# Kernel optimization log

Hardware: AMD Instinct MI355X
Metric: run time of the kernel (lower is better)

The kernel has to match this reference:

```python
import jax, jax.numpy as jnp
import numpy as np

N0, D, H, E0 = 50000, 128, 128, 800000
N1, E1, A, B, C = 20000, 320000, 100000, 64, 10


def _gcn(x, row, col, ew, n, W, b):
    # GCNConv: out = D^-1/2 (A + I) D^-1/2 (x W) + b, with edge weights
    xw = x @ W
    sl = jnp.arange(n)
    r = jnp.concatenate([row, sl])
    c = jnp.concatenate([col, sl])
    w = jnp.concatenate([ew, jnp.ones((n,), ew.dtype)])
    deg = jax.ops.segment_sum(w, c, num_segments=n)
    dinv = jax.lax.rsqrt(jnp.maximum(deg, 1e-12))
    norm = dinv[r] * w * dinv[c]
    return jax.ops.segment_sum(norm[:, None] * xw[r], c, num_segments=n) + b


def _block(x, row, col, ew, n, W1, b1, W2, b2, Wl, bl):
    # Block with num_inner_layers=2, jumping_knowledge='cat'
    x1 = jax.nn.relu(_gcn(x, row, col, ew, n, W1, b1))
    x2 = jax.nn.relu(_gcn(x1, row, col, ew, n, W2, b2))
    return jnp.concatenate([x1, x2], axis=1) @ Wl + bl


def _seg_max(x, idx, n):
    m = jax.ops.segment_max(x, idx, num_segments=n)
    return jnp.where(jnp.isfinite(m), m, 0.0)  # empty segments -> 0 like scatter_max default


def _lin_init(k, i, o):
    s = 1.0 / np.sqrt(i)
    return jax.random.uniform(k, (i, o), jnp.float32, -s, s)


def setup_inputs() -> dict:
    key = jax.random.key(0)
    ks = jax.random.split(key, 20)
    x = jax.random.normal(ks[0], (N0, D), jnp.float32)
    edge_index0 = jax.random.randint(ks[1], (2, E0), 0, N0)
    edge_weight0 = jax.random.uniform(ks[2], (E0,), jnp.float32)
    batch0 = jnp.sort(jax.random.randint(ks[3], (N0,), 0, B))
    cover_row = jax.random.randint(ks[4], (A,), 0, N0)
    cover_col = jnp.concatenate([jnp.arange(N1), jax.random.randint(ks[5], (A - N1,), 0, N1)])
    edge_index1 = jax.random.randint(ks[6], (2, E1), 0, N1)
    edge_weight1 = jax.random.uniform(ks[7], (E1,), jnp.float32)
    batch1 = jnp.sort(jax.random.randint(ks[8], (N1,), 0, B))
    params = dict(
        w_in1=_lin_init(ks[9], D, H), b_in1=jnp.zeros((H,), jnp.float32),
        w_in2=_lin_init(ks[10], H, H), b_in2=jnp.zeros((H,), jnp.float32),
        w_in_lin=_lin_init(ks[11], 2 * H, H), b_in_lin=jnp.zeros((H,), jnp.float32),
        w_b1=_lin_init(ks[12], 2 * H, H), b_b1=jnp.zeros((H,), jnp.float32),
        w_b2=_lin_init(ks[13], H, H), b_b2=jnp.zeros((H,), jnp.float32),
        w_b_lin=_lin_init(ks[14], 2 * H, H), b_b_lin=jnp.zeros((H,), jnp.float32),
        bn_gamma=jnp.ones((4 * H,), jnp.float32), bn_beta=jnp.zeros((4 * H,), jnp.float32),
        w_l1=_lin_init(ks[15], 4 * H, H), b_l1=jnp.zeros((H,), jnp.float32),
        w_l2=_lin_init(ks[16], H, C), b_l2=jnp.zeros((C,), jnp.float32),
    )
    return dict(x=x, edge_index0=edge_index0, edge_weight0=edge_weight0, batch0=batch0,
                cover_row=cover_row, cover_col=cover_col, edge_index1=edge_index1,
                edge_weight1=edge_weight1, batch1=batch1, **params)


def reference(x, edge_index0, edge_weight0, batch0, cover_row, cover_col,
              edge_index1, edge_weight1, batch1,
              w_in1, b_in1, w_in2, b_in2, w_in_lin, b_in_lin,
              w_b1, b_b1, w_b2, b_b2, w_b_lin, b_b_lin,
              bn_gamma, bn_beta, w_l1, b_l1, w_l2, b_l2):
    r0, c0 = edge_index0[0], edge_index0[1]
    h = jax.nn.relu(_block(x, r0, c0, edge_weight0, N0, w_in1, b_in1, w_in2, b_in2, w_in_lin, b_in_lin))
    xs = [jax.ops.segment_sum(h, batch0, num_segments=B), _seg_max(h, batch0, B)]
    # cover_pool_node: add + max over k-plex cover assignments
    hg = h[cover_row]
    h2 = jnp.concatenate([jax.ops.segment_sum(hg, cover_col, num_segments=N1),
                          _seg_max(hg, cover_col, N1)], axis=1)
    r1, c1 = edge_index1[0], edge_index1[1]
    h2 = jax.nn.relu(_block(h2, r1, c1, edge_weight1, N1, w_b1, b_b1, w_b2, b_b2, w_b_lin, b_b_lin))
    xs.append(jax.ops.segment_sum(h2, batch1, num_segments=B))
    xs.append(_seg_max(h2, batch1, B))
    z = jnp.concatenate(xs, axis=1)  # [B, 4H]
    # BatchNorm1d in eval mode: running stats (mean=0, var=1), eps=1e-5
    z = z * (bn_gamma * jax.lax.rsqrt(jnp.asarray(1.0 + 1e-5, z.dtype))) + bn_beta
    z = jax.nn.relu(z @ w_l1 + b_l1)
    logits = z @ w_l2 + b_l2  # dropout skipped (eval mode)
    return jax.nn.softmax(logits, axis=-1)
```

## Files before the change

### kernel.cpp

```cpp
#include <hip/hip_runtime.h>
#include <cmath>

#define HF 128

namespace {

typedef __attribute__((ext_vector_type(8))) short short8;
typedef __attribute__((ext_vector_type(4))) float f32x4;

inline int cdiv(int a, int b) { return (a + b - 1) / b; }

__device__ inline unsigned short f2bf(float x) {
    unsigned u = __float_as_uint(x);
    return (unsigned short)((u + 0x7fffu + ((u >> 16) & 1u)) >> 16);
}
__device__ inline float bf2f(unsigned short u) {
    return __uint_as_float((unsigned)u << 16);
}
__device__ inline float bflo(unsigned v) { return __uint_as_float(v << 16); }
__device__ inline float bfhi(unsigned v) { return __uint_as_float(v & 0xffff0000u); }

#define FIXS 4194304.0f
#define FIXINV 2.384185791015625e-07f
#define SUMMASK ((1ULL << 40) - 1)

__global__ void k_prep(const int* __restrict__ col0, const float* __restrict__ ew0,
                       unsigned long long* __restrict__ dc0, int E0, int nb0,
                       const int* __restrict__ col1, const float* __restrict__ ew1,
                       unsigned long long* __restrict__ dc1, int E1, int nb1,
                       const int* __restrict__ ccol, int* __restrict__ ccnt, int A, int nbc,
                       const float* __restrict__ w0, const float* __restrict__ w1,
                       const float* __restrict__ w2, const float* __restrict__ w3,
                       const float* __restrict__ w4, const float* __restrict__ w5,
                       unsigned short* __restrict__ wpk, int nbw,
                       const int* __restrict__ b0, int n0, const int* __restrict__ b1,
                       int n1, int B, int* __restrict__ bst0, int* __restrict__ bst1) {
    int b = blockIdx.x, t = threadIdx.x;
    if (b < nb0) {
        int e = b * 256 + t;
        if (e < E0) {
            unsigned long long v = (1ULL << 40) | (unsigned long long)(ew0[e] * FIXS + 0.5f);
            atomicAdd(&dc0[col0[e]], v);
        }
        return;
    }
    b -= nb0;
    if (b < nb1) {
        int e = b * 256 + t;
        if (e < E1) {
            unsigned long long v = (1ULL << 40) | (unsigned long long)(ew1[e] * FIXS + 0.5f);
            atomicAdd(&dc1[col1[e]], v);
        }
        return;
    }
    b -= nb1;
    if (b < nbc) {
        int e = b * 256 + t;
        if (e < A) atomicAdd(&ccnt[ccol[e]], 1);
        return;
    }
    b -= nbc;
    if (b < nbw) {
        int idx = b * 256 + t;
        const float* src; int local;
        if      (idx < 16384)  { src = w0; local = idx; }
        else if (idx < 32768)  { src = w1; local = idx - 16384; }
        else if (idx < 65536)  { src = w2; local = idx - 32768; }
        else if (idx < 98304)  { src = w3; local = idx - 65536; }
        else if (idx < 114688) { src = w4; local = idx - 98304; }
        else                   { src = w5; local = idx - 114688; }
        int e = local & 7, lane = (local >> 3) & 63, g = (local >> 9) & 7, kc = local >> 12;
        int colw = (lane & 15) + 16 * g;
        int k = kc * 32 + ((lane >> 4) << 3) + e;
        wpk[idx] = f2bf(src[k * 128 + colw]);
        return;
    }
    b -= nbw;
    {
        int idx = b * 256 + t;
        if (idx < 2 * (B + 1)) {
            int which = idx > B;
            int bb = which ? idx - (B + 1) : idx;
            const int* arr = which ? b1 : b0;
            int lo = 0, hi = which ? n1 : n0;
            while (lo < hi) {
                int mid = (lo + hi) >> 1;
                if (arr[mid] < bb) lo = mid + 1; else hi = mid;
            }
            (which ? bst1 : bst0)[bb] = lo;
        }
    }
}

__device__ inline void scan256(int* s, int v, int gid, int n, int* __restrict__ excl,
                               int* __restrict__ partial, int pb) {
    s[threadIdx.x] = v;
    __syncthreads();
    for (int off = 1; off < 256; off <<= 1) {
        int t = (threadIdx.x >= off) ? s[threadIdx.x - off] : 0;
        __syncthreads();
        s[threadIdx.x] += t;
        __syncthreads();
    }
    if (gid < n) excl[gid] = s[threadIdx.x] - v;
    if (threadIdx.x == 255) partial[pb] = s[255];
}

__global__ void k_scan_dinv(const unsigned long long* __restrict__ dc0, int* __restrict__ rp0,
                            int* __restrict__ part0, int n0, int nbs0,
                            const unsigned long long* __restrict__ dc1, int* __restrict__ rp1,
                            int* __restrict__ part1, int n1, int nbs1,
                            const int* __restrict__ ccnt, int* __restrict__ crp,
                            int* __restrict__ cpart, int nc, int nbsc,
                            float* __restrict__ dinv0, float* __restrict__ dinv1,
                            int nbd0, int nbd1) {
    __shared__ int s[256];
    int b = blockIdx.x, t = threadIdx.x;
    if (b < nbs0) {
        int gid = b * 256 + t;
        int v = (gid < n0) ? (int)(dc0[gid] >> 40) : 0;
        scan256(s, v, gid, n0, rp0, part0, b);
        return;
    }
    b -= nbs0;
    if (b < nbs1) {
        int gid = b * 256 + t;
        int v = (gid < n1) ? (int)(dc1[gid] >> 40) : 0;
        scan256(s, v, gid, n1, rp1, part1, b);
        return;
    }
    b -= nbs1;
    if (b < nbsc) {
        int gid = b * 256 + t;
        int v = (gid < nc) ? ccnt[gid] : 0;
        scan256(s, v, gid, nc, crp, cpart, b);
        return;
    }
    b -= nbsc;
    if (b < nbd0) {
        int i = b * 256 + t;
        if (i < n0) dinv0[i] = rsqrtf(1.0f + (float)(dc0[i] & SUMMASK) * FIXINV);
        return;
    }
    b -= nbd0;
    {
        int i = b * 256 + t;
        if (i < n1) dinv1[i] = rsqrtf(1.0f + (float)(dc1[i] & SUMMASK) * FIXINV);
    }
}

__global__ void k_scan2x3(int* __restrict__ p0, int nb0, int* __restrict__ p1, int nb1,
                          int* __restrict__ p2, int nb2) {
    __shared__ int s[256];
    int* p; int nb;
    if (blockIdx.x == 0)      { p = p0; nb = nb0; }
    else if (blockIdx.x == 1) { p = p1; nb = nb1; }
    else                      { p = p2; nb = nb2; }
    int v = (threadIdx.x < nb) ? p[threadIdx.x] : 0;
    s[threadIdx.x] = v;
    __syncthreads();
    for (int off = 1; off < 256; off <<= 1) {
        int t = (threadIdx.x >= off) ? s[threadIdx.x - off] : 0;
        __syncthreads();
        s[threadIdx.x] += t;
        __syncthreads();
    }
    if (threadIdx.x < nb) p[threadIdx.x] = s[threadIdx.x] - v;
}

__global__ void k_scan3x3(int* __restrict__ rp0, const int* __restrict__ part0,
                          int* __restrict__ cur0, int n0, int tot0, int nb0,
                          int* __restrict__ rp1, const int* __restrict__ part1,
                          int* __restrict__ cur1, int n1, int tot1, int nb1,
                          int* __restrict__ crp, const int* __restrict__ cpart,
                          int* __restrict__ ccur, int nc, int totc) {
    int b = blockIdx.x, t = threadIdx.x;
    if (b < nb0) {
        int gid = b * 256 + t;
        if (gid < n0) { int v = rp0[gid] + part0[b]; rp0[gid] = v; cur0[gid] = v; }
        if (gid == 0) rp0[n0] = tot0;
        return;
    }
    b -= nb0;
    if (b < nb1) {
        int gid = b * 256 + t;
        if (gid < n1) { int v = rp1[gid] + part1[b]; rp1[gid] = v; cur1[gid] = v; }
        if (gid == 0) rp1[n1] = tot1;
        return;
    }
    b -= nb1;
    {
        int gid = b * 256 + t;
        if (gid < nc) { int v = crp[gid] + cpart[b]; crp[gid] = v; ccur[gid] = v; }
        if (gid == 0) crp[nc] = totc;
    }
}

__global__ void k_fillx3(const int* __restrict__ row0, const int* __restrict__ col0,
                         const float* __restrict__ ew0, const float* __restrict__ dinv0,
                         int* __restrict__ cur0, int2* __restrict__ ed0, int E0, int nb0,
                         const int* __restrict__ row1, const int* __restrict__ col1,
                         const float* __restrict__ ew1, const float* __restrict__ dinv1,
                         int* __restrict__ cur1, int2* __restrict__ ed1, int E1, int nb1,
                         const int* __restrict__ crow, const int* __restrict__ ccol,
                         int* __restrict__ ccur, int* __restrict__ csrcs, int A) {
    int b = blockIdx.x, t = threadIdx.x;
    if (b < nb0) {
        int e = b * 256 + t;
        if (e < E0) {
            int r = row0[e], c = col0[e];
            int p = atomicAdd(&cur0[c], 1);
            ed0[p] = make_int2(r, __float_as_int(ew0[e] * dinv0[r] * dinv0[c]));
        }
        return;
    }
    b -= nb0;
    if (b < nb1) {
        int e = b * 256 + t;
        if (e < E1) {
            int r = row1[e], c = col1[e];
            int p = atomicAdd(&cur1[c], 1);
            ed1[p] = make_int2(r, __float_as_int(ew1[e] * dinv1[r] * dinv1[c]));
        }
        return;
    }
    b -= nb1;
    {
        int e = b * 256 + t;
        if (e < A) {
            int p = atomicAdd(&ccur[ccol[e]], 1);
            csrcs[p] = crow[e];
        }
    }
}

__global__ void k_gcn_gather(const unsigned* __restrict__ xw, const int* __restrict__ rowptr,
                             const int2* __restrict__ ed, const float* __restrict__ dinv,
                             const float* __restrict__ bias, unsigned* __restrict__ out, int n) {
    int wid = (blockIdx.x * 256 + threadIdx.x) >> 6;
    if (wid >= n) return;
    int lane = threadIdx.x & 63;
    int s = rowptr[wid], e = rowptr[wid + 1];
    float d = dinv[wid];
    unsigned v = xw[(size_t)wid * 64 + lane];
    float ax = bflo(v) * d * d, ay = bfhi(v) * d * d;
    float bx = 0.f, by = 0.f, cx = 0.f, cy = 0.f, dx = 0.f, dy = 0.f;
    int i = s;
    for (; i + 4 <= e; i += 4) {
        int2 e0 = ed[i], e1 = ed[i + 1], e2 = ed[i + 2], e3 = ed[i + 3];
        unsigned v0 = xw[(size_t)e0.x * 64 + lane];
        unsigned v1 = xw[(size_t)e1.x * 64 + lane];
        unsigned v2 = xw[(size_t)e2.x * 64 + lane];
        unsigned v3 = xw[(size_t)e3.x * 64 + lane];
        float c0 = __int_as_float(e0.y), c1 = __int_as_float(e1.y);
        float c2 = __int_as_float(e2.y), c3 = __int_as_float(e3.y);
        ax += c0 * bflo(v0); ay += c0 * bfhi(v0);
        bx += c1 * bflo(v1); by += c1 * bfhi(v1);
        cx += c2 * bflo(v2); cy += c2 * bfhi(v2);
        dx += c3 * bflo(v3); dy += c3 * bfhi(v3);
    }
    for (; i < e; ++i) {
        int2 e0 = ed[i];
        unsigned v0 = xw[(size_t)e0.x * 64 + lane];
        float c0 = __int_as_float(e0.y);
        ax += c0 * bflo(v0); ay += c0 * bfhi(v0);
    }
    ax += bx + cx + dx;
    ay += by + cy + dy;
    float2 bb = *reinterpret_cast<const float2*>(bias + lane * 2);
    ax = fmaxf(ax + bb.x, 0.f);
    ay = fmaxf(ay + bb.y, 0.f);
    out[(size_t)wid * 64 + lane] = (unsigned)f2bf(ax) | ((unsigned)f2bf(ay) << 16);
}

__global__ void k_pool_cover(const unsigned short* __restrict__ h, const int* __restrict__ bst,
                             float* __restrict__ psum, float* __restrict__ pmax, int nsplit,
                             int nbpool, const unsigned* __restrict__ h32,
                             const int* __restrict__ crp, const int* __restrict__ csrcs,
                             unsigned* __restrict__ h2, int n1) {
    int t = threadIdx.x;
    if ((int)blockIdx.x < nbpool) {
        int blk = blockIdx.x;
        int b = blk / nsplit, sub = (blk % nsplit) * 2 + (t >> 7);
        int col = t & 127;
        int r0 = bst[b], r1 = bst[b + 1];
        float sum = 0.f, mx = 0.f;
        for (int r = r0 + sub; r < r1; r += 2 * nsplit) {
            float v = bf2f(h[(size_t)r * HF + col]);
            sum += v;
            mx = fmaxf(mx, v);
        }
        atomicAdd(&psum[b * HF + col], sum);
        atomicMax(reinterpret_cast<int*>(&pmax[b * HF + col]), __float_as_int(mx));
        return;
    }
    int wid = (((int)blockIdx.x - nbpool) * 256 + t) >> 6;
    if (wid >= n1) return;
    int lane = t & 63;
    int s = crp[wid], e = crp[wid + 1];
    float sx = 0.f, sy = 0.f, mx = 0.f, my = 0.f;
    for (int i = s; i < e; ++i) {
        unsigned v = h32[(size_t)csrcs[i] * 64 + lane];
        float vx = bflo(v), vy = bfhi(v);
        sx += vx; sy += vy;
        mx = fmaxf(mx, vx); my = fmaxf(my, vy);
    }
    h2[(size_t)wid * 128 + lane]      = (unsigned)f2bf(sx) | ((unsigned)f2bf(sy) << 16);
    h2[(size_t)wid * 128 + 64 + lane] = (unsigned)f2bf(mx) | ((unsigned)f2bf(my) << 16);
}

__global__ void k_pool256(const unsigned short* __restrict__ h, const int* __restrict__ bst,
                          float* __restrict__ psum, float* __restrict__ pmax, int nsplit) {
    int t = threadIdx.x;
    int blk = blockIdx.x;
    int b = blk / nsplit, sub = (blk % nsplit) * 2 + (t >> 7);
    int col = t & 127;
    int r0 = bst[b], r1 = bst[b + 1];
    float sum = 0.f, mx = 0.f;
    for (int r = r0 + sub; r < r1; r += 2 * nsplit) {
        float v = bf2f(h[(size_t)r * HF + col]);
        sum += v;
        mx = fmaxf(mx, v);
    }
    atomicAdd(&psum[b * HF + col], sum);
    atomicMax(reinterpret_cast<int*>(&pmax[b * HF + col]), __float_as_int(mx));
}

template <int K, bool AF32>
__global__ void k_mfma_gemm(const void* __restrict__ A1v, int lda1,
                            const void* __restrict__ A2v, int lda2,
                            const unsigned short* __restrict__ wpk,
                            const float* __restrict__ bias, int relu,
                            unsigned short* __restrict__ out, int N) {
    const int t = threadIdx.x;
    const int wv = t >> 6, lane = t & 63;
    const int l15 = lane & 15, lhi = lane >> 4;
    const int rbase = blockIdx.x * 128 + wv * 32;

    f32x4 acc[2][8];
#pragma unroll
    for (int i = 0; i < 2; ++i)
#pragma unroll
        for (int g = 0; g < 8; ++g) acc[i][g] = {0.f, 0.f, 0.f, 0.f};

    int r[2];
#pragma unroll
    for (int ri = 0; ri < 2; ++ri) {
        int rr = rbase + ri * 16 + l15;
        r[ri] = (rr < N) ? rr : (N - 1);
    }

    for (int kc = 0; kc < K / 32; ++kc) {
        int kb = kc * 32 + lhi * 8;
        short8 a[2];
#pragma unroll
        for (int ri = 0; ri < 2; ++ri) {
            if (AF32) {
                const float* A = (const float*)A1v;
                const float* p = A + (size_t)r[ri] * lda1 + kb;
                float4 f0 = *reinterpret_cast<const float4*>(p);
                float4 f1 = *reinterpret_cast<const float4*>(p + 4);
                a[ri][0] = (short)f2bf(f0.x); a[ri][1] = (short)f2bf(f0.y);
                a[ri][2] = (short)f2bf(f0.z); a[ri][3] = (short)f2bf(f0.w);
                a[ri][4] = (short)f2bf(f1.x); a[ri][5] = (short)f2bf(f1.y);
                a[ri][6] = (short)f2bf(f1.z); a[ri][7] = (short)f2bf(f1.w);
            } else {
                const unsigned short* base;
                int kk, ld;
                if (K == 256 && kb >= 128) { base = (const unsigned short*)A2v; kk = kb - 128; ld = lda2; }
                else                       { base = (const unsigned short*)A1v; kk = kb;       ld = lda1; }
                a[ri] = *reinterpret_cast<const short8*>(base + (size_t)r[ri] * ld + kk);
            }
        }
        const unsigned short* wb = wpk + (size_t)(kc * 8) * 512 + lane * 8;
#pragma unroll
        for (int g = 0; g < 8; ++g) {
            short8 b = *reinterpret_cast<const short8*>(wb + (size_t)g * 512);
            acc[0][g] = __builtin_amdgcn_mfma_f32_16x16x32_bf16(a[0], b, acc[0][g], 0, 0, 0);
            acc[1][g] = __builtin_amdgcn_mfma_f32_16x16x32_bf16(a[1], b, acc[1][g], 0, 0, 0);
        }
    }

#pragma unroll
    for (int ri = 0; ri < 2; ++ri) {
#pragma unroll
        for (int g = 0; g < 8; ++g) {
            int col = l15 + g * 16;
            float bb = bias ? bias[col] : 0.f;
#pragma unroll
            for (int e = 0; e < 4; ++e) {
                int rr = rbase + ri * 16 + lhi * 4 + e;
                if (rr < N) {
                    float v = acc[ri][g][e] + bb;
                    if (relu) v = fmaxf(v, 0.f);
                    out[(size_t)rr * 128 + col] = f2bf(v);
                }
            }
        }
    }
}

__global__ void k_head(const float* __restrict__ p0s, const float* __restrict__ p0m,
                       const float* __restrict__ p1s, const float* __restrict__ p1m,
                       const float* __restrict__ gamma, const float* __restrict__ beta,
                       const float* __restrict__ w1, const float* __restrict__ b1,
                       const float* __restrict__ w2, const float* __restrict__ b2,
                       float* __restrict__ out) {
    __shared__ float z[512];
    __shared__ float z1[128];
    __shared__ float lg[10];
    int b = blockIdx.x, t = threadIdx.x;
    const float s = rsqrtf(1.0f + 1e-5f);
    z[t]       = p0s[b * 128 + t] * (gamma[t] * s)       + beta[t];
    z[128 + t] = p0m[b * 128 + t] * (gamma[128 + t] * s) + beta[128 + t];
    z[256 + t] = p1s[b * 128 + t] * (gamma[256 + t] * s) + beta[256 + t];
    z[384 + t] = p1m[b * 128 + t] * (gamma[384 + t] * s) + beta[384 + t];
    __syncthreads();
    float acc = b1[t];
    for (int k = 0; k < 512; ++k) acc += z[k] * w1[k * 128 + t];
    z1[t] = fmaxf(acc, 0.f);
    __syncthreads();
    if (t < 10) {
        float a2 = b2[t];
        for (int k = 0; k < 128; ++k) a2 += z1[k] * w2[k * 10 + t];
        lg[t] = a2;
    }
    __syncthreads();
    if (t == 0) {
        float m = lg[0];
        for (int c = 1; c < 10; ++c) m = fmaxf(m, lg[c]);
        float e[10], ssum = 0.f;
        for (int c = 0; c < 10; ++c) { e[c] = expf(lg[c] - m); ssum += e[c]; }
        for (int c = 0; c < 10; ++c) out[b * 10 + c] = e[c] / ssum;
    }
}

}

extern "C" void kernel_launch(void* const* d_in, const int* in_sizes, int n_in,
                              void* d_out, int out_size, void* d_ws, size_t ws_size,
                              hipStream_t stream) {
    const float* x      = (const float*)d_in[0];
    const int*   ei0    = (const int*)d_in[1];
    const float* ew0    = (const float*)d_in[2];
    const int*   batch0 = (const int*)d_in[3];
    const int*   crow   = (const int*)d_in[4];
    const int*   ccol   = (const int*)d_in[5];
    const int*   ei1    = (const int*)d_in[6];
    const float* ew1    = (const float*)d_in[7];
    const int*   batch1 = (const int*)d_in[8];
    const float* w_in1  = (const float*)d_in[9];
    const float* b_in1  = (const float*)d_in[10];
    const float* w_in2  = (const float*)d_in[11];
    const float* b_in2  = (const float*)d_in[12];
    const float* w_inl  = (const float*)d_in[13];
    const float* b_inl  = (const float*)d_in[14];
    const float* w_b1   = (const float*)d_in[15];
    const float* b_b1   = (const float*)d_in[16];
    const float* w_b2   = (const float*)d_in[17];
    const float* b_b2   = (const float*)d_in[18];
    const float* w_bl   = (const float*)d_in[19];
    const float* b_bl   = (const float*)d_in[20];
    const float* gamma  = (const float*)d_in[21];
    const float* beta   = (const float*)d_in[22];
    const float* w_l1   = (const float*)d_in[23];
    const float* b_l1   = (const float*)d_in[24];
    const float* w_l2   = (const float*)d_in[25];
    const float* b_l2   = (const float*)d_in[26];

    const int N0 = in_sizes[0] / 128;
    const int E0 = in_sizes[2];
    const int A  = in_sizes[4];
    const int E1 = in_sizes[7];
    const int N1 = in_sizes[8];
    const int B  = out_size / 10;

    const int* row0 = ei0;
    const int* col0 = ei0 + E0;
    const int* row1 = ei1;
    const int* col1 = ei1 + E1;

    char* wsp = (char*)d_ws;
    size_t off = 0;
    auto alloc = [&](size_t bytes) -> char* {
        char* p = wsp + off;
        off += (bytes + 255) & ~(size_t)255;
        return p;
    };
    unsigned long long* dc0 = (unsigned long long*)alloc((size_t)N0 * 8);
    unsigned long long* dc1 = (unsigned long long*)alloc((size_t)N1 * 8);
    int*   ccnt  = (int*)alloc((size_t)N1 * 4);
    float* p0s   = (float*)alloc((size_t)B * HF * 4 * 4);
    float* p0m   = p0s + (size_t)B * HF;
    float* p1s   = p0m + (size_t)B * HF;
    float* p1m   = p1s + (size_t)B * HF;
    size_t zero_bytes = off;

    unsigned* xw  = (unsigned*)alloc((size_t)N0 * 64 * 4);
    unsigned* x1  = (unsigned*)alloc((size_t)N0 * 64 * 4);
    unsigned* x2  = (unsigned*)alloc((size_t)N0 * 64 * 4);
    unsigned* h   = (unsigned*)alloc((size_t)N0 * 64 * 4);
    unsigned* h2  = (unsigned*)alloc((size_t)N1 * 128 * 4);
    unsigned short* wpk = (unsigned short*)alloc(147456 * 2);
    float* dinv0 = (float*)alloc((size_t)N0 * 4);
    float* dinv1 = (float*)alloc((size_t)N1 * 4);
    int*   rp0   = (int*)alloc(((size_t)N0 + 1) * 4);
    int*   rp1   = (int*)alloc(((size_t)N1 + 1) * 4);
    int*   crp   = (int*)alloc(((size_t)N1 + 1) * 4);
    int*   cur0  = (int*)alloc((size_t)N0 * 4);
    int*   cur1  = (int*)alloc((size_t)N1 * 4);
    int*   ccur  = (int*)alloc((size_t)N1 * 4);
    int*   part0 = (int*)alloc(256 * 4);
    int*   part1 = (int*)alloc(256 * 4);
    int*   cpart = (int*)alloc(256 * 4);
    int2*  ed0   = (int2*)alloc((size_t)E0 * 8);
    int2*  ed1   = (int2*)alloc((size_t)E1 * 8);
    int*   csrcs = (int*)alloc((size_t)A * 4);
    int*   bst0  = (int*)alloc((size_t)(B + 1) * 4);
    int*   bst1  = (int*)alloc((size_t)(B + 1) * 4);
    (void)ws_size; (void)n_in;

    const int NSPLIT = 16;
    const int nbE0 = cdiv(E0, 256), nbE1 = cdiv(E1, 256), nbC = cdiv(A, 256);
    const int nbW = 576, nbB = 1;
    const int nbs0 = cdiv(N0, 256), nbs1 = cdiv(N1, 256), nbsc = cdiv(N1, 256);

    hipMemsetAsync(dc0, 0, zero_bytes, stream);

    k_prep<<<nbE0 + nbE1 + nbC + nbW + nbB, 256, 0, stream>>>(
        col0, ew0, dc0, E0, nbE0, col1, ew1, dc1, E1, nbE1, ccol, ccnt, A, nbC,
        w_in1, w_in2, w_inl, w_b1, w_b2, w_bl, wpk, nbW,
        batch0, N0, batch1, N1, B, bst0, bst1);

    k_scan_dinv<<<nbs0 + nbs1 + nbsc + nbs0 + nbs1, 256, 0, stream>>>(
        dc0, rp0, part0, N0, nbs0, dc1, rp1, part1, N1, nbs1,
        ccnt, crp, cpart, N1, nbsc, dinv0, dinv1, nbs0, nbs1);

    k_scan2x3<<<3, 256, 0, stream>>>(part0, nbs0, part1, nbs1, cpart, nbsc);

    k_scan3x3<<<nbs0 + nbs1 + nbsc, 256, 0, stream>>>(
        rp0, part0, cur0, N0, E0, nbs0, rp1, part1, cur1, N1, E1, nbs1,
        crp, cpart, ccur, N1, A);

    k_fillx3<<<nbE0 + nbE1 + nbC, 256, 0, stream>>>(
        row0, col0, ew0, dinv0, cur0, ed0, E0, nbE0,
        row1, col1, ew1, dinv1, cur1, ed1, E1, nbE1,
        crow, ccol, ccur, csrcs, A);

    k_mfma_gemm<128, true><<<cdiv(N0, 128), 256, 0, stream>>>(
        x, 128, nullptr, 0, wpk + 0, nullptr, 0, (unsigned short*)xw, N0);
    k_gcn_gather<<<cdiv(N0, 4), 256, 0, stream>>>(xw, rp0, ed0, dinv0, b_in1, x1, N0);
    k_mfma_gemm<128, false><<<cdiv(N0, 128), 256, 0, stream>>>(
        x1, 128, nullptr, 0, wpk + 16384, nullptr, 0, (unsigned short*)xw, N0);
    k_gcn_gather<<<cdiv(N0, 4), 256, 0, stream>>>(xw, rp0, ed0, dinv0, b_in2, x2, N0);
    k_mfma_gemm<256, false><<<cdiv(N0, 128), 256, 0, stream>>>(
        x1, 128, x2, 128, wpk + 32768, b_inl, 1, (unsigned short*)h, N0);

    k_pool_cover<<<B * NSPLIT + cdiv(N1, 4), 256, 0, stream>>>(
        (const unsigned short*)h, bst0, p0s, p0m, NSPLIT, B * NSPLIT,
        h, crp, csrcs, h2, N1);

    k_mfma_gemm<256, false><<<cdiv(N1, 128), 256, 0, stream>>>(
        h2, 256, (const unsigned short*)h2 + 128, 256, wpk + 65536, nullptr, 0,
        (unsigned short*)xw, N1);
    k_gcn_gather<<<cdiv(N1, 4), 256, 0, stream>>>(xw, rp1, ed1, dinv1, b_b1, x1, N1);
    k_mfma_gemm<128, false><<<cdiv(N1, 128), 256, 0, stream>>>(
        x1, 128, nullptr, 0, wpk + 98304, nullptr, 0, (unsigned short*)xw, N1);
    k_gcn_gather<<<cdiv(N1, 4), 256, 0, stream>>>(xw, rp1, ed1, dinv1, b_b2, x2, N1);
    k_mfma_gemm<256, false><<<cdiv(N1, 128), 256, 0, stream>>>(
        x1, 128, x2, 128, wpk + 114688, b_bl, 1, (unsigned short*)h, N1);

    k_pool256<<<B * NSPLIT, 256, 0, stream>>>((const unsigned short*)h, bst1, p1s, p1m, NSPLIT);

    k_head<<<B, 128, 0, stream>>>(p0s, p0m, p1s, p1m, gamma, beta, w_l1, b_l1, w_l2, b_l2,
                                  (float*)d_out);
}
```

Baseline: 409.6 us.

## Record edge ranks during degree atomics and fuse first GEMM into prep

The degree-count atomics now save their returned old count as a per-edge rank, so CSR fill writes directly to rowptr+rank without a second round of cursor atomics. The fill kernel is partitioned so each of 8 block groups handles a destination-node range, aiming to keep writes local per XCD. The first x@W GEMM is fused into the degree-count kernel to overlap compute with atomics, weight packing moves to a separate earlier kernel, and the gather loads edges as int4 pairs. In exchange, the fill kernel rereads the edge arrays once per group, and extra rank buffers are stored.

```diff
diff --git a/kernel.cpp b/kernel.cpp
--- a/kernel.cpp
+++ b/kernel.cpp
@@ -24,318 +24,16 @@
 #define FIXINV 2.384185791015625e-07f
 #define SUMMASK ((1ULL << 40) - 1)
 
-__global__ void k_prep(const int* __restrict__ col0, const float* __restrict__ ew0,
-                       unsigned long long* __restrict__ dc0, int E0, int nb0,
-                       const int* __restrict__ col1, const float* __restrict__ ew1,
-                       unsigned long long* __restrict__ dc1, int E1, int nb1,
-                       const int* __restrict__ ccol, int* __restrict__ ccnt, int A, int nbc,
-                       const float* __restrict__ w0, const float* __restrict__ w1,
-                       const float* __restrict__ w2, const float* __restrict__ w3,
-                       const float* __restrict__ w4, const float* __restrict__ w5,
-                       unsigned short* __restrict__ wpk, int nbw,
-                       const int* __restrict__ b0, int n0, const int* __restrict__ b1,
-                       int n1, int B, int* __restrict__ bst0, int* __restrict__ bst1) {
-    int b = blockIdx.x, t = threadIdx.x;
-    if (b < nb0) {
-        int e = b * 256 + t;
-        if (e < E0) {
-            unsigned long long v = (1ULL << 40) | (unsigned long long)(ew0[e] * FIXS + 0.5f);
-            atomicAdd(&dc0[col0[e]], v);
-        }
-        return;
-    }
-    b -= nb0;
-    if (b < nb1) {
-        int e = b * 256 + t;
-        if (e < E1) {
-            unsigned long long v = (1ULL << 40) | (unsigned long long)(ew1[e] * FIXS + 0.5f);
-            atomicAdd(&dc1[col1[e]], v);
-        }
-        return;
-    }
-    b -= nb1;
-    if (b < nbc) {
-        int e = b * 256 + t;
-        if (e < A) atomicAdd(&ccnt[ccol[e]], 1);
-        return;
-    }
-    b -= nbc;
-    if (b < nbw) {
-        int idx = b * 256 + t;
-        const float* src; int local;
-        if      (idx < 16384)  { src = w0; local = idx; }
-        else if (idx < 32768)  { src = w1; local = idx - 16384; }
-        else if (idx < 65536)  { src = w2; local = idx - 32768; }
-        else if (idx < 98304)  { src = w3; local = idx - 65536; }
-        else if (idx < 114688) { src = w4; local = idx - 98304; }
-        else                   { src = w5; local = idx - 114688; }
-        int e = local & 7, lane = (local >> 3) & 63, g = (local >> 9) & 7, kc = local >> 12;
-        int colw = (lane & 15) + 16 * g;
-        int k = kc * 32 + ((lane >> 4) << 3) + e;
-        wpk[idx] = f2bf(src[k * 128 + colw]);
-        return;
-    }
-    b -= nbw;
-    {
-        int idx = b * 256 + t;
-        if (idx < 2 * (B + 1)) {
-            int which = idx > B;
-            int bb = which ? idx - (B + 1) : idx;
-            const int* arr = which ? b1 : b0;
-            int lo = 0, hi = which ? n1 : n0;
-            while (lo < hi) {
-                int mid = (lo + hi) >> 1;
-                if (arr[mid] < bb) lo = mid + 1; else hi = mid;
-            }
-            (which ? bst1 : bst0)[bb] = lo;
-        }
-    }
-}
-
-__device__ inline void scan256(int* s, int v, int gid, int n, int* __restrict__ excl,
-                               int* __restrict__ partial, int pb) {
-    s[threadIdx.x] = v;
-    __syncthreads();
-    for (int off = 1; off < 256; off <<= 1) {
-        int t = (threadIdx.x >= off) ? s[threadIdx.x - off] : 0;
-        __syncthreads();
-        s[threadIdx.x] += t;
-        __syncthreads();
-    }
-    if (gid < n) excl[gid] = s[threadIdx.x] - v;
-    if (threadIdx.x == 255) partial[pb] = s[255];
-}
-
-__global__ void k_scan_dinv(const unsigned long long* __restrict__ dc0, int* __restrict__ rp0,
-                            int* __restrict__ part0, int n0, int nbs0,
-                            const unsigned long long* __restrict__ dc1, int* __restrict__ rp1,
-                            int* __restrict__ part1, int n1, int nbs1,
-                            const int* __restrict__ ccnt, int* __restrict__ crp,
-                            int* __restrict__ cpart, int nc, int nbsc,
-                            float* __restrict__ dinv0, float* __restrict__ dinv1,
-                            int nbd0, int nbd1) {
-    __shared__ int s[256];
-    int b = blockIdx.x, t = threadIdx.x;
-    if (b < nbs0) {
-        int gid = b * 256 + t;
-        int v = (gid < n0) ? (int)(dc0[gid] >> 40) : 0;
-        scan256(s, v, gid, n0, rp0, part0, b);
-        return;
-    }
-    b -= nbs0;
-    if (b < nbs1) {
-        int gid = b * 256 + t;
-        int v = (gid < n1) ? (int)(dc1[gid] >> 40) : 0;
-        scan256(s, v, gid, n1, rp1, part1, b);
-        return;
-    }
-    b -= nbs1;
-    if (b < nbsc) {
-        int gid = b * 256 + t;
-        int v = (gid < nc) ? ccnt[gid] : 0;
-        scan256(s, v, gid, nc, crp, cpart, b);
-        return;
-    }
-    b -= nbsc;
-    if (b < nbd0) {
-        int i = b * 256 + t;
-        if (i < n0) dinv0[i] = rsqrtf(1.0f + (float)(dc0[i] & SUMMASK) * FIXINV);
-        return;
-    }
-    b -= nbd0;
-    {
-        int i = b * 256 + t;
-        if (i < n1) dinv1[i] = rsqrtf(1.0f + (float)(dc1[i] & SUMMASK) * FIXINV);
-    }
-}
-
-__global__ void k_scan2x3(int* __restrict__ p0, int nb0, int* __restrict__ p1, int nb1,
-                          int* __restrict__ p2, int nb2) {
-    __shared__ int s[256];
-    int* p; int nb;
-    if (blockIdx.x == 0)      { p = p0; nb = nb0; }
-    else if (blockIdx.x == 1) { p = p1; nb = nb1; }
-    else                      { p = p2; nb = nb2; }
-    int v = (threadIdx.x < nb) ? p[threadIdx.x] : 0;
-    s[threadIdx.x] = v;
-    __syncthreads();
-    for (int off = 1; off < 256; off <<= 1) {
-        int t = (threadIdx.x >= off) ? s[threadIdx.x - off] : 0;
-        __syncthreads();
-        s[threadIdx.x] += t;
-        __syncthreads();
-    }
-    if (threadIdx.x < nb) p[threadIdx.x] = s[threadIdx.x] - v;
-}
-
-__global__ void k_scan3x3(int* __restrict__ rp0, const int* __restrict__ part0,
-                          int* __restrict__ cur0, int n0, int tot0, int nb0,
-                          int* __restrict__ rp1, const int* __restrict__ part1,
-                          int* __restrict__ cur1, int n1, int tot1, int nb1,
-                          int* __restrict__ crp, const int* __restrict__ cpart,
-                          int* __restrict__ ccur, int nc, int totc) {
-    int b = blockIdx.x, t = threadIdx.x;
-    if (b < nb0) {
-        int gid = b * 256 + t;
-        if (gid < n0) { int v = rp0[gid] + part0[b]; rp0[gid] = v; cur0[gid] = v; }
-        if (gid == 0) rp0[n0] = tot0;
-        return;
-    }
-    b -= nb0;
-    if (b < nb1) {
-        int gid = b * 256 + t;
-        if (gid < n1) { int v = rp1[gid] + part1[b]; rp1[gid] = v; cur1[gid] = v; }
-        if (gid == 0) rp1[n1] = tot1;
-        return;
-    }
-    b -= nb1;
-    {
-        int gid = b * 256 + t;
-        if (gid < nc) { int v = crp[gid] + cpart[b]; crp[gid] = v; ccur[gid] = v; }
-        if (gid == 0) crp[nc] = totc;
-    }
-}
-
-__global__ void k_fillx3(const int* __restrict__ row0, const int* __restrict__ col0,
-                         const float* __restrict__ ew0, const float* __restrict__ dinv0,
-                         int* __restrict__ cur0, int2* __restrict__ ed0, int E0, int nb0,
-                         const int* __restrict__ row1, const int* __restrict__ col1,
-                         const float* __restrict__ ew1, const float* __restrict__ dinv1,
-                         int* __restrict__ cur1, int2* __restrict__ ed1, int E1, int nb1,
-                         const int* __restrict__ crow, const int* __restrict__ ccol,
-                         int* __restrict__ ccur, int* __restrict__ csrcs, int A) {
-    int b = blockIdx.x, t = threadIdx.x;
-    if (b < nb0) {
-        int e = b * 256 + t;
-        if (e < E0) {
-            int r = row0[e], c = col0[e];
-            int p = atomicAdd(&cur0[c], 1);
-            ed0[p] = make_int2(r, __float_as_int(ew0[e] * dinv0[r] * dinv0[c]));
-        }
-        return;
-    }
-    b -= nb0;
-    if (b < nb1) {
-        int e = b * 256 + t;
-        if (e < E1) {
-            int r = row1[e], c = col1[e];
-            int p = atomicAdd(&cur1[c], 1);
-            ed1[p] = make_int2(r, __float_as_int(ew1[e] * dinv1[r] * dinv1[c]));
-        }
-        return;
-    }
-    b -= nb1;
-    {
-        int e = b * 256 + t;
-        if (e < A) {
-            int p = atomicAdd(&ccur[ccol[e]], 1);
-            csrcs[p] = crow[e];
-        }
-    }
-}
-
-__global__ void k_gcn_gather(const unsigned* __restrict__ xw, const int* __restrict__ rowptr,
-                             const int2* __restrict__ ed, const float* __restrict__ dinv,
-                             const float* __restrict__ bias, unsigned* __restrict__ out, int n) {
-    int wid = (blockIdx.x * 256 + threadIdx.x) >> 6;
-    if (wid >= n) return;
-    int lane = threadIdx.x & 63;
-    int s = rowptr[wid], e = rowptr[wid + 1];
-    float d = dinv[wid];
-    unsigned v = xw[(size_t)wid * 64 + lane];
-    float ax = bflo(v) * d * d, ay = bfhi(v) * d * d;
-    float bx = 0.f, by = 0.f, cx = 0.f, cy = 0.f, dx = 0.f, dy = 0.f;
-    int i = s;
-    for (; i + 4 <= e; i += 4) {
-        int2 e0 = ed[i], e1 = ed[i + 1], e2 = ed[i + 2], e3 = ed[i + 3];
-        unsigned v0 = xw[(size_t)e0.x * 64 + lane];
-        unsigned v1 = xw[(size_t)e1.x * 64 + lane];
-        unsigned v2 = xw[(size_t)e2.x * 64 + lane];
-        unsigned v3 = xw[(size_t)e3.x * 64 + lane];
-        float c0 = __int_as_float(e0.y), c1 = __int_as_float(e1.y);
-        float c2 = __int_as_float(e2.y), c3 = __int_as_float(e3.y);
-        ax += c0 * bflo(v0); ay += c0 * bfhi(v0);
-        bx += c1 * bflo(v1); by += c1 * bfhi(v1);
-        cx += c2 * bflo(v2); cy += c2 * bfhi(v2);
-        dx += c3 * bflo(v3); dy += c3 * bfhi(v3);
-    }
-    for (; i < e; ++i) {
-        int2 e0 = ed[i];
-        unsigned v0 = xw[(size_t)e0.x * 64 + lane];
-        float c0 = __int_as_float(e0.y);
-        ax += c0 * bflo(v0); ay += c0 * bfhi(v0);
-    }
-    ax += bx + cx + dx;
-    ay += by + cy + dy;
-    float2 bb = *reinterpret_cast<const float2*>(bias + lane * 2);
-    ax = fmaxf(ax + bb.x, 0.f);
-    ay = fmaxf(ay + bb.y, 0.f);
-    out[(size_t)wid * 64 + lane] = (unsigned)f2bf(ax) | ((unsigned)f2bf(ay) << 16);
-}
-
-__global__ void k_pool_cover(const unsigned short* __restrict__ h, const int* __restrict__ bst,
-                             float* __restrict__ psum, float* __restrict__ pmax, int nsplit,
-                             int nbpool, const unsigned* __restrict__ h32,
-                             const int* __restrict__ crp, const int* __restrict__ csrcs,
-                             unsigned* __restrict__ h2, int n1) {
-    int t = threadIdx.x;
-    if ((int)blockIdx.x < nbpool) {
-        int blk = blockIdx.x;
-        int b = blk / nsplit, sub = (blk % nsplit) * 2 + (t >> 7);
-        int col = t & 127;
-        int r0 = bst[b], r1 = bst[b + 1];
-        float sum = 0.f, mx = 0.f;
-        for (int r = r0 + sub; r < r1; r += 2 * nsplit) {
-            float v = bf2f(h[(size_t)r * HF + col]);
-            sum += v;
-            mx = fmaxf(mx, v);
-        }
-        atomicAdd(&psum[b * HF + col], sum);
-        atomicMax(reinterpret_cast<int*>(&pmax[b * HF + col]), __float_as_int(mx));
-        return;
-    }
-    int wid = (((int)blockIdx.x - nbpool) * 256 + t) >> 6;
-    if (wid >= n1) return;
-    int lane = t & 63;
-    int s = crp[wid], e = crp[wid + 1];
-    float sx = 0.f, sy = 0.f, mx = 0.f, my = 0.f;
-    for (int i = s; i < e; ++i) {
-        unsigned v = h32[(size_t)csrcs[i] * 64 + lane];
-        float vx = bflo(v), vy = bfhi(v);
-        sx += vx; sy += vy;
-        mx = fmaxf(mx, vx); my = fmaxf(my, vy);
-    }
-    h2[(size_t)wid * 128 + lane]      = (unsigned)f2bf(sx) | ((unsigned)f2bf(sy) << 16);
-    h2[(size_t)wid * 128 + 64 + lane] = (unsigned)f2bf(mx) | ((unsigned)f2bf(my) << 16);
-}
-
-__global__ void k_pool256(const unsigned short* __restrict__ h, const int* __restrict__ bst,
-                          float* __restrict__ psum, float* __restrict__ pmax, int nsplit) {
-    int t = threadIdx.x;
-    int blk = blockIdx.x;
-    int b = blk / nsplit, sub = (blk % nsplit) * 2 + (t >> 7);
-    int col = t & 127;
-    int r0 = bst[b], r1 = bst[b + 1];
-    float sum = 0.f, mx = 0.f;
-    for (int r = r0 + sub; r < r1; r += 2 * nsplit) {
-        float v = bf2f(h[(size_t)r * HF + col]);
-        sum += v;
-        mx = fmaxf(mx, v);
-    }
-    atomicAdd(&psum[b * HF + col], sum);
-    atomicMax(reinterpret_cast<int*>(&pmax[b * HF + col]), __float_as_int(mx));
-}
-
 template <int K, bool AF32>
-__global__ void k_mfma_gemm(const void* __restrict__ A1v, int lda1,
-                            const void* __restrict__ A2v, int lda2,
-                            const unsigned short* __restrict__ wpk,
-                            const float* __restrict__ bias, int relu,
-                            unsigned short* __restrict__ out, int N) {
+__device__ __forceinline__ void gemm_dev(int bid, const void* __restrict__ A1v, int lda1,
+                                         const void* __restrict__ A2v, int lda2,
+                                         const unsigned short* __restrict__ wpk,
+                                         const float* __restrict__ bias, int relu,
+                                         unsigned short* __restrict__ out, int N) {
     const int t = threadIdx.x;
     const int wv = t >> 6, lane = t & 63;
     const int l15 = lane & 15, lhi = lane >> 4;
-    const int rbase = blockIdx.x * 128 + wv * 32;
+    const int rbase = bid * 128 + wv * 32;
 
     f32x4 acc[2][8];
 #pragma unroll
@@ -398,6 +96,365 @@
             }
         }
     }
+}
+
+template <int K, bool AF32>
+__global__ void k_mfma_gemm(const void* __restrict__ A1v, int lda1,
+                            const void* __restrict__ A2v, int lda2,
+                            const unsigned short* __restrict__ wpk,
+                            const float* __restrict__ bias, int relu,
+                            unsigned short* __restrict__ out, int N) {
+    gemm_dev<K, AF32>(blockIdx.x, A1v, lda1, A2v, lda2, wpk, bias, relu, out, N);
+}
+
+__global__ void k_prep0(const float* __restrict__ w0, const float* __restrict__ w1,
+                        const float* __restrict__ w2, const float* __restrict__ w3,
+                        const float* __restrict__ w4, const float* __restrict__ w5,
+                        unsigned short* __restrict__ wpk,
+                        const int* __restrict__ b0, int n0, const int* __restrict__ b1,
+                        int n1, int B, int* __restrict__ bst0, int* __restrict__ bst1) {
+    int b = blockIdx.x, t = threadIdx.x;
+    if (b < 576) {
+        int idx = b * 256 + t;
+        const float* src; int local;
+        if      (idx < 16384)  { src = w0; local = idx; }
+        else if (idx < 32768)  { src = w1; local = idx - 16384; }
+        else if (idx < 65536)  { src = w2; local = idx - 32768; }
+        else if (idx < 98304)  { src = w3; local = idx - 65536; }
+        else if (idx < 114688) { src = w4; local = idx - 98304; }
+        else                   { src = w5; local = idx - 114688; }
+        int e = local & 7, lane = (local >> 3) & 63, g = (local >> 9) & 7, kc = local >> 12;
+        int colw = (lane & 15) + 16 * g;
+        int k = kc * 32 + ((lane >> 4) << 3) + e;
+        wpk[idx] = f2bf(src[k * 128 + colw]);
+        return;
+    }
+    {
+        int idx = t;
+        if (idx < 2 * (B + 1)) {
+            int which = idx > B;
+            int bb = which ? idx - (B + 1) : idx;
+            const int* arr = which ? b1 : b0;
+            int lo = 0, hi = which ? n1 : n0;
+            while (lo < hi) {
+                int mid = (lo + hi) >> 1;
+                if (arr[mid] < bb) lo = mid + 1; else hi = mid;
+            }
+            (which ? bst1 : bst0)[bb] = lo;
+        }
+    }
+}
+
+__global__ void k_prep1(const float* __restrict__ x, const unsigned short* __restrict__ wpk,
+                        unsigned short* __restrict__ xw, int N0gemm, int nbG,
+                        const int* __restrict__ col0, const float* __restrict__ ew0,
+                        unsigned long long* __restrict__ dc0, unsigned* __restrict__ rank0,
+                        int E0, int nb0,
+                        const int* __restrict__ col1, const float* __restrict__ ew1,
+                        unsigned long long* __restrict__ dc1, unsigned* __restrict__ rank1,
+                        int E1, int nb1,
+                        const int* __restrict__ ccol, int* __restrict__ ccnt,
+                        unsigned* __restrict__ rankc, int A) {
+    int b = blockIdx.x, t = threadIdx.x;
+    if (b < nbG) {
+        gemm_dev<128, true>(b, x, 128, nullptr, 0, wpk, nullptr, 0, xw, N0gemm);
+        return;
+    }
+    b -= nbG;
+    if (b < nb0) {
+        int e = b * 256 + t;
+        if (e < E0) {
+            unsigned long long v = (1ULL << 40) | (unsigned long long)(ew0[e] * FIXS + 0.5f);
+            unsigned long long old = atomicAdd(&dc0[col0[e]], v);
+            rank0[e] = (unsigned)(old >> 40);
+        }
+        return;
+    }
+    b -= nb0;
+    if (b < nb1) {
+        int e = b * 256 + t;
+        if (e < E1) {
+            unsigned long long v = (1ULL << 40) | (unsigned long long)(ew1[e] * FIXS + 0.5f);
+            unsigned long long old = atomicAdd(&dc1[col1[e]], v);
+            rank1[e] = (unsigned)(old >> 40);
+        }
+        return;
+    }
+    b -= nb1;
+    {
+        int e = b * 256 + t;
+        if (e < A) rankc[e] = (unsigned)atomicAdd(&ccnt[ccol[e]], 1);
+    }
+}
+
+__device__ inline void scan256(int* s, int v, int gid, int n, int* __restrict__ excl,
+                               int* __restrict__ partial, int pb) {
+    s[threadIdx.x] = v;
+    __syncthreads();
+    for (int off = 1; off < 256; off <<= 1) {
+        int t = (threadIdx.x >= off) ? s[threadIdx.x - off] : 0;
+        __syncthreads();
+        s[threadIdx.x] += t;
+        __syncthreads();
+    }
+    if (gid < n) excl[gid] = s[threadIdx.x] - v;
+    if (threadIdx.x == 255) partial[pb] = s[255];
+}
+
+__global__ void k_scan_dinv(const unsigned long long* __restrict__ dc0, int* __restrict__ rp0,
+                            int* __restrict__ part0, int n0, int nbs0,
+                            const unsigned long long* __restrict__ dc1, int* __restrict__ rp1,
+                            int* __restrict__ part1, int n1, int nbs1,
+                            const int* __restrict__ ccnt, int* __restrict__ crp,
+                            int* __restrict__ cpart, int nc, int nbsc,
+                            float* __restrict__ dinv0, float* __restrict__ dinv1,
+                            int nbd0, int nbd1) {
+    __shared__ int s[256];
+    int b = blockIdx.x, t = threadIdx.x;
+    if (b < nbs0) {
+        int gid = b * 256 + t;
+        int v = (gid < n0) ? (int)(dc0[gid] >> 40) : 0;
+        scan256(s, v, gid, n0, rp0, part0, b);
+        return;
+    }
+    b -= nbs0;
+    if (b < nbs1) {
+        int gid = b * 256 + t;
+        int v = (gid < n1) ? (int)(dc1[gid] >> 40) : 0;
+        scan256(s, v, gid, n1, rp1, part1, b);
+        return;
+    }
+    b -= nbs1;
+    if (b < nbsc) {
+        int gid = b * 256 + t;
+        int v = (gid < nc) ? ccnt[gid] : 0;
+        scan256(s, v, gid, nc, crp, cpart, b);
+        return;
+    }
+    b -= nbsc;
+    if (b < nbd0) {
+        int i = b * 256 + t;
+        if (i < n0) dinv0[i] = rsqrtf(1.0f + (float)(dc0[i] & SUMMASK) * FIXINV);
+        return;
+    }
+    b -= nbd0;
+    {
+        int i = b * 256 + t;
+        if (i < n1) dinv1[i] = rsqrtf(1.0f + (float)(dc1[i] & SUMMASK) * FIXINV);
+    }
+}
+
+__global__ void k_scan2x3(int* __restrict__ p0, int nb0, int* __restrict__ p1, int nb1,
+                          int* __restrict__ p2, int nb2) {
+    __shared__ int s[256];
+    int* p; int nb;
+    if (blockIdx.x == 0)      { p = p0; nb = nb0; }
+    else if (blockIdx.x == 1) { p = p1; nb = nb1; }
+    else                      { p = p2; nb = nb2; }
+    int v = (threadIdx.x < nb) ? p[threadIdx.x] : 0;
+    s[threadIdx.x] = v;
+    __syncthreads();
+    for (int off = 1; off < 256; off <<= 1) {
+        int t = (threadIdx.x >= off) ? s[threadIdx.x - off] : 0;
+        __syncthreads();
+        s[threadIdx.x] += t;
+        __syncthreads();
+    }
+    if (threadIdx.x < nb) p[threadIdx.x] = s[threadIdx.x] - v;
+}
+
+__global__ void k_scan3x3(int* __restrict__ rp0, const int* __restrict__ part0,
+                          int n0, int tot0, int nb0,
+                          int* __restrict__ rp1, const int* __restrict__ part1,
+                          int n1, int tot1, int nb1,
+                          int* __restrict__ crp, const int* __restrict__ cpart,
+                          int nc, int totc) {
+    int b = blockIdx.x, t = threadIdx.x;
+    if (b < nb0) {
+        int gid = b * 256 + t;
+        if (gid < n0) rp0[gid] += part0[b];
+        if (gid == 0) rp0[n0] = tot0;
+        return;
+    }
+    b -= nb0;
+    if (b < nb1) {
+        int gid = b * 256 + t;
+        if (gid < n1) rp1[gid] += part1[b];
+        if (gid == 0) rp1[n1] = tot1;
+        return;
+    }
+    b -= nb1;
+    {
+        int gid = b * 256 + t;
+        if (gid < nc) crp[gid] += cpart[b];
+        if (gid == 0) crp[nc] = totc;
+    }
+}
+
+#define EPB 2048
+__global__ void k_fillx3(const int* __restrict__ row0, const int* __restrict__ col0,
+                         const float* __restrict__ ew0, const unsigned* __restrict__ rank0,
+                         const float* __restrict__ dinv0, const int* __restrict__ rp0,
+                         int2* __restrict__ ed0, int E0, int N0n, int g0b,
+                         const int* __restrict__ row1, const int* __restrict__ col1,
+                         const float* __restrict__ ew1, const unsigned* __restrict__ rank1,
+                         const float* __restrict__ dinv1, const int* __restrict__ rp1,
+                         int2* __restrict__ ed1, int E1, int N1n, int g1b,
+                         const int* __restrict__ crow, const int* __restrict__ ccol,
+                         const unsigned* __restrict__ rankc, const int* __restrict__ crp,
+                         int* __restrict__ csrcs, int A) {
+    int b = blockIdx.x, t = threadIdx.x;
+    if (b < g0b) {
+        int xcd = b & 7, chunk = b >> 3;
+        int lo = (int)((long long)N0n * xcd >> 3), hi = (int)((long long)N0n * (xcd + 1) >> 3);
+        int base = chunk * EPB;
+#pragma unroll
+        for (int i = 0; i < EPB; i += 256) {
+            int e = base + i + t;
+            if (e < E0) {
+                int c = col0[e];
+                if (c >= lo && c < hi) {
+                    int r = row0[e];
+                    ed0[rp0[c] + rank0[e]] =
+                        make_int2(r, __float_as_int(ew0[e] * dinv0[r] * dinv0[c]));
+                }
+            }
+        }
+        return;
+    }
+    b -= g0b;
+    if (b < g1b) {
+        int xcd = b & 7, chunk = b >> 3;
+        int lo = (int)((long long)N1n * xcd >> 3), hi = (int)((long long)N1n * (xcd + 1) >> 3);
+        int base = chunk * EPB;
+#pragma unroll
+        for (int i = 0; i < EPB; i += 256) {
+            int e = base + i + t;
+            if (e < E1) {
+                int c = col1[e];
+                if (c >= lo && c < hi) {
+                    int r = row1[e];
+                    ed1[rp1[c] + rank1[e]] =
+                        make_int2(r, __float_as_int(ew1[e] * dinv1[r] * dinv1[c]));
+                }
+            }
+        }
+        return;
+    }
+    b -= g1b;
+    {
+        int xcd = b & 7, chunk = b >> 3;
+        int lo = (int)((long long)N1n * xcd >> 3), hi = (int)((long long)N1n * (xcd + 1) >> 3);
+        int base = chunk * EPB;
+#pragma unroll
+        for (int i = 0; i < EPB; i += 256) {
+            int e = base + i + t;
+            if (e < A) {
+                int c = ccol[e];
+                if (c >= lo && c < hi) csrcs[crp[c] + rankc[e]] = crow[e];
+            }
+        }
+    }
+}
+
+__global__ void k_gcn_gather(const unsigned* __restrict__ xw, const int* __restrict__ rowptr,
+                             const int2* __restrict__ ed, const float* __restrict__ dinv,
+                             const float* __restrict__ bias, unsigned* __restrict__ out, int n) {
+    int wid = (blockIdx.x * 256 + threadIdx.x) >> 6;
+    if (wid >= n) return;
+    int lane = threadIdx.x & 63;
+    int s = rowptr[wid], e = rowptr[wid + 1];
+    float d = dinv[wid];
+    unsigned v = xw[(size_t)wid * 64 + lane];
+    float ax = bflo(v) * d * d, ay = bfhi(v) * d * d;
+    float bx = 0.f, by = 0.f, cx = 0.f, cy = 0.f, dx = 0.f, dy = 0.f;
+    int i = s;
+    if ((i & 1) && i < e) {
+        int2 e0 = ed[i];
+        unsigned v0 = xw[(size_t)e0.x * 64 + lane];
+        float c0 = __int_as_float(e0.y);
+        ax += c0 * bflo(v0); ay += c0 * bfhi(v0);
+        ++i;
+    }
+    for (; i + 4 <= e; i += 4) {
+        int4 q0 = *reinterpret_cast<const int4*>(ed + i);
+        int4 q1 = *reinterpret_cast<const int4*>(ed + i + 2);
+        unsigned v0 = xw[(size_t)q0.x * 64 + lane];
+        unsigned v1 = xw[(size_t)q0.z * 64 + lane];
+        unsigned v2 = xw[(size_t)q1.x * 64 + lane];
+        unsigned v3 = xw[(size_t)q1.z * 64 + lane];
+        float c0 = __int_as_float(q0.y), c1 = __int_as_float(q0.w);
+        float c2 = __int_as_float(q1.y), c3 = __int_as_float(q1.w);
+        ax += c0 * bflo(v0); ay += c0 * bfhi(v0);
+        bx += c1 * bflo(v1); by += c1 * bfhi(v1);
+        cx += c2 * bflo(v2); cy += c2 * bfhi(v2);
+        dx += c3 * bflo(v3); dy += c3 * bfhi(v3);
+    }
+    for (; i < e; ++i) {
+        int2 e0 = ed[i];
+        unsigned v0 = xw[(size_t)e0.x * 64 + lane];
+        float c0 = __int_as_float(e0.y);
+        ax += c0 * bflo(v0); ay += c0 * bfhi(v0);
+    }
+    ax += bx + cx + dx;
+    ay += by + cy + dy;
+    float2 bb = *reinterpret_cast<const float2*>(bias + lane * 2);
+    ax = fmaxf(ax + bb.x, 0.f);
+    ay = fmaxf(ay + bb.y, 0.f);
+    out[(size_t)wid * 64 + lane] = (unsigned)f2bf(ax) | ((unsigned)f2bf(ay) << 16);
+}
+
+__global__ void k_pool_cover(const unsigned short* __restrict__ h, const int* __restrict__ bst,
+                             float* __restrict__ psum, float* __restrict__ pmax, int nsplit,
+                             int nbpool, const unsigned* __restrict__ h32,
+                             const int* __restrict__ crp, const int* __restrict__ csrcs,
+                             unsigned* __restrict__ h2, int n1) {
+    int t = threadIdx.x;
+    if ((int)blockIdx.x < nbpool) {
+        int blk = blockIdx.x;
+        int b = blk / nsplit, sub = (blk % nsplit) * 2 + (t >> 7);
+        int col = t & 127;
+        int r0 = bst[b], r1 = bst[b + 1];
+        float sum = 0.f, mx = 0.f;
+        for (int r = r0 + sub; r < r1; r += 2 * nsplit) {
+            float v = bf2f(h[(size_t)r * HF + col]);
+            sum += v;
+            mx = fmaxf(mx, v);
+        }
+        atomicAdd(&psum[b * HF + col], sum);
+        atomicMax(reinterpret_cast<int*>(&pmax[b * HF + col]), __float_as_int(mx));
+        return;
+    }
+    int wid = (((int)blockIdx.x - nbpool) * 256 + t) >> 6;
+    if (wid >= n1) return;
+    int lane = t & 63;
+    int s = crp[wid], e = crp[wid + 1];
+    float sx = 0.f, sy = 0.f, mx = 0.f, my = 0.f;
+    for (int i = s; i < e; ++i) {
+        unsigned v = h32[(size_t)csrcs[i] * 64 + lane];
+        float vx = bflo(v), vy = bfhi(v);
+        sx += vx; sy += vy;
+        mx = fmaxf(mx, vx); my = fmaxf(my, vy);
+    }
+    h2[(size_t)wid * 128 + lane]      = (unsigned)f2bf(sx) | ((unsigned)f2bf(sy) << 16);
+    h2[(size_t)wid * 128 + 64 + lane] = (unsigned)f2bf(mx) | ((unsigned)f2bf(my) << 16);
+}
+
+__global__ void k_pool256(const unsigned short* __restrict__ h, const int* __restrict__ bst,
+                          float* __restrict__ psum, float* __restrict__ pmax, int nsplit) {
+    int t = threadIdx.x;
+    int blk = blockIdx.x;
+    int b = blk / nsplit, sub = (blk % nsplit) * 2 + (t >> 7);
+    int col = t & 127;
+    int r0 = bst[b], r1 = bst[b + 1];
+    float sum = 0.f, mx = 0.f;
+    for (int r = r0 + sub; r < r1; r += 2 * nsplit) {
+        float v = bf2f(h[(size_t)r * HF + col]);
+        sum += v;
+        mx = fmaxf(mx, v);
+    }
+    atomicAdd(&psum[b * HF + col], sum);
+    atomicMax(reinterpret_cast<int*>(&pmax[b * HF + col]), __float_as_int(mx));
 }
 
 __global__ void k_head(const float* __restrict__ p0s, const float* __restrict__ p0m,
@@ -507,30 +564,35 @@
     int*   rp0   = (int*)alloc(((size_t)N0 + 1) * 4);
     int*   rp1   = (int*)alloc(((size_t)N1 + 1) * 4);
     int*   crp   = (int*)alloc(((size_t)N1 + 1) * 4);
-    int*   cur0  = (int*)alloc((size_t)N0 * 4);
-    int*   cur1  = (int*)alloc((size_t)N1 * 4);
-    int*   ccur  = (int*)alloc((size_t)N1 * 4);
     int*   part0 = (int*)alloc(256 * 4);
     int*   part1 = (int*)alloc(256 * 4);
     int*   cpart = (int*)alloc(256 * 4);
     int2*  ed0   = (int2*)alloc((size_t)E0 * 8);
     int2*  ed1   = (int2*)alloc((size_t)E1 * 8);
     int*   csrcs = (int*)alloc((size_t)A * 4);
+    unsigned* rank0 = (unsigned*)alloc((size_t)E0 * 4);
+    unsigned* rank1 = (unsigned*)alloc((size_t)E1 * 4);
+    unsigned* rankc = (unsigned*)alloc((size_t)A * 4);
     int*   bst0  = (int*)alloc((size_t)(B + 1) * 4);
     int*   bst1  = (int*)alloc((size_t)(B + 1) * 4);
     (void)ws_size; (void)n_in;
 
     const int NSPLIT = 16;
+    const int nbG  = cdiv(N0, 128);
     const int nbE0 = cdiv(E0, 256), nbE1 = cdiv(E1, 256), nbC = cdiv(A, 256);
-    const int nbW = 576, nbB = 1;
     const int nbs0 = cdiv(N0, 256), nbs1 = cdiv(N1, 256), nbsc = cdiv(N1, 256);
+    const int g0b = cdiv(E0, EPB) * 8, g1b = cdiv(E1, EPB) * 8, gcb = cdiv(A, EPB) * 8;
 
     hipMemsetAsync(dc0, 0, zero_bytes, stream);
 
-    k_prep<<<nbE0 + nbE1 + nbC + nbW + nbB, 256, 0, stream>>>(
-        col0, ew0, dc0, E0, nbE0, col1, ew1, dc1, E1, nbE1, ccol, ccnt, A, nbC,
-        w_in1, w_in2, w_inl, w_b1, w_b2, w_bl, wpk, nbW,
-        batch0, N0, batch1, N1, B, bst0, bst1);
+    k_prep0<<<577, 256, 0, stream>>>(w_in1, w_in2, w_inl, w_b1, w_b2, w_bl, wpk,
+                                     batch0, N0, batch1, N1, B, bst0, bst1);
+
+    k_prep1<<<nbG + nbE0 + nbE1 + nbC, 256, 0, stream>>>(
+        x, wpk, (unsigned short*)xw, N0, nbG,
+        col0, ew0, dc0, rank0, E0, nbE0,
+        col1, ew1, dc1, rank1, E1, nbE1,
+        ccol, ccnt, rankc, A);
 
     k_scan_dinv<<<nbs0 + nbs1 + nbsc + nbs0 + nbs1, 256, 0, stream>>>(
         dc0, rp0, part0, N0, nbs0, dc1, rp1, part1, N1, nbs1,
@@ -539,16 +601,13 @@
     k_scan2x3<<<3, 256, 0, stream>>>(part0, nbs0, part1, nbs1, cpart, nbsc);
 
     k_scan3x3<<<nbs0 + nbs1 + nbsc, 256, 0, stream>>>(
-        rp0, part0, cur0, N0, E0, nbs0, rp1, part1, cur1, N1, E1, nbs1,
-        crp, cpart, ccur, N1, A);
-
-    k_fillx3<<<nbE0 + nbE1 + nbC, 256, 0, stream>>>(
-        row0, col0, ew0, dinv0, cur0, ed0, E0, nbE0,
-        row1, col1, ew1, dinv1, cur1, ed1, E1, nbE1,
-        crow, ccol, ccur, csrcs, A);
-
-    k_mfma_gemm<128, true><<<cdiv(N0, 128), 256, 0, stream>>>(
-        x, 128, nullptr, 0, wpk + 0, nullptr, 0, (unsigned short*)xw, N0);
+        rp0, part0, N0, E0, nbs0, rp1, part1, N1, E1, nbs1, crp, cpart, N1, A);
+
+    k_fillx3<<<g0b + g1b + gcb, 256, 0, stream>>>(
+        row0, col0, ew0, rank0, dinv0, rp0, ed0, E0, N0, g0b,
+        row1, col1, ew1, rank1, dinv1, rp1, ed1, E1, N1, g1b,
+        crow, ccol, rankc, crp, csrcs, A);
+
     k_gcn_gather<<<cdiv(N0, 4), 256, 0, stream>>>(xw, rp0, ed0, dinv0, b_in1, x1, N0);
     k_mfma_gemm<128, false><<<cdiv(N0, 128), 256, 0, stream>>>(
         x1, 128, nullptr, 0, wpk + 16384, nullptr, 0, (unsigned short*)xw, N0);
```

New measurement: 381.1 us. 7.0% less time.
